# Kernel tuning notes

Measured on AMD Instinct MI355X. Metric: run time of the kernel, lower is better.

Reference implementation:

```python
import jax, jax.numpy as jnp
import numpy as np

N0, N1, N2 = 360448, 22528, 2048
E0, E1 = 337920, 20480
D = 256


def setup_inputs() -> dict:
    key = jax.random.key(0)
    ks = jax.random.split(key, 12)
    s = 1.0 / np.sqrt(D)
    return {
        "x": jax.random.normal(ks[0], (N0, D), dtype=jnp.float32),
        "src0": jax.random.randint(ks[1], (E0,), 0, N0, dtype=jnp.int32),
        "dst0": jax.random.randint(ks[2], (E0,), 0, N1, dtype=jnp.int32),
        "src1": jax.random.randint(ks[3], (E1,), 0, N1, dtype=jnp.int32),
        "dst1": jax.random.randint(ks[4], (E1,), 0, N2, dtype=jnp.int32),
        "Wl0": jax.random.normal(ks[5], (D, D), dtype=jnp.float32) * s,
        "bl0": jnp.zeros((D,), dtype=jnp.float32),
        "Wr0": jax.random.normal(ks[6], (D, D), dtype=jnp.float32) * s,
        "Wl1": jax.random.normal(ks[7], (D, D), dtype=jnp.float32) * s,
        "bl1": jnp.zeros((D,), dtype=jnp.float32),
        "Wr1": jax.random.normal(ks[8], (D, D), dtype=jnp.float32) * s,
    }


def _sage_conv(x_src, x_tgt, src, dst, n_tgt, Wl, bl, Wr):
    # mean aggregation of source neighbor features per target node
    summed = jax.ops.segment_sum(x_src[src], dst, num_segments=n_tgt)
    cnt = jax.ops.segment_sum(jnp.ones((src.shape[0],), x_src.dtype), dst,
                              num_segments=n_tgt)
    agg = summed / jnp.maximum(cnt, 1.0)[:, None]
    # PyG SAGEConv: lin_l(agg) + lin_r(x_target); lin_r has no bias
    return agg @ Wl.T + bl + x_tgt @ Wr.T


def reference(x, src0, dst0, src1, dst1, Wl0, bl0, Wr0, Wl1, bl1, Wr1):
    # layer 0: [N0, D] -> [N1, D]
    h = _sage_conv(x, x[:N1], src0, dst0, N1, Wl0, bl0, Wr0)
    h = jax.nn.relu(h)  # dropout is identity in eval mode
    # layer 1: [N1, D] -> [N2, D]
    out = _sage_conv(h, h[:N2], src1, dst1, N2, Wl1, bl1, Wr1)
    return out
```

## Files before the change

### kernel.cpp

```cpp
#include <hip/hip_runtime.h>
#include <hip/hip_bf16.h>

#define N1C 22528
#define N2C 2048

typedef __attribute__((ext_vector_type(8))) short bf16x8;
typedef __attribute__((ext_vector_type(4))) float f32x4;

__device__ __forceinline__ short f2bf(float f) {
    union { float f; unsigned u; } x; x.f = f;
    unsigned r = x.u + 0x7fff + ((x.u >> 16) & 1);
    return (short)(r >> 16);
}
__device__ __forceinline__ float bf2f(unsigned short u) {
    union { unsigned u; float f; } x; x.u = ((unsigned)u) << 16;
    return x.f;
}

__global__ void prep_kernel(const float* __restrict__ Wl0, const float* __restrict__ Wr0,
                            const float* __restrict__ Wl1, const float* __restrict__ Wr1,
                            short* __restrict__ Wcat0, short* __restrict__ Wcat1,
                            int* __restrict__ hist0, int* __restrict__ hist1) {
    const int stride = gridDim.x * blockDim.x;
    const int tid0 = blockIdx.x * blockDim.x + threadIdx.x;
    for (int i = tid0; i < 2 * 256 * 512; i += stride) {
        int layer = i >> 17;
        int r = i & ((1 << 17) - 1);
        int j = r >> 9, k = r & 511;
        const float* Wl = layer ? Wl1 : Wl0;
        const float* Wr = layer ? Wr1 : Wr0;
        float v = (k < 256) ? Wl[j * 256 + k] : Wr[j * 256 + (k - 256)];
        (layer ? Wcat1 : Wcat0)[r] = f2bf(v);
    }
    for (int i = tid0; i < N1C + N2C; i += stride) {
        if (i < N1C) hist0[i] = 0; else hist1[i - N1C] = 0;
    }
}

__global__ void hist_both_kernel(const int* __restrict__ dst0, int E0,
                                 const int* __restrict__ dst1, int E1,
                                 int* __restrict__ hist0, int* __restrict__ hist1) {
    const int stride = gridDim.x * blockDim.x;
    for (int i = blockIdx.x * blockDim.x + threadIdx.x; i < E0 + E1; i += stride) {
        if (i < E0) atomicAdd(&hist0[dst0[i]], 1);
        else        atomicAdd(&hist1[dst1[i - E0]], 1);
    }
}

__global__ __launch_bounds__(1024)
void scan_both_kernel(const int* __restrict__ hist0, int* __restrict__ rowptr0,
                      int* __restrict__ cursor0,
                      const int* __restrict__ hist1, int* __restrict__ rowptr1,
                      int* __restrict__ cursor1) {
    __shared__ int sums[1024];
    const int N = (blockIdx.x == 0) ? N1C : N2C;
    const int* hist   = (blockIdx.x == 0) ? hist0 : hist1;
    int* rowptr       = (blockIdx.x == 0) ? rowptr0 : rowptr1;
    int* cursor       = (blockIdx.x == 0) ? cursor0 : cursor1;
    const int tid = threadIdx.x;
    const int per = (N + 1023) >> 10;
    const int start = tid * per;
    const int end = min(start + per, N);
    int s = 0;
    for (int i = start; i < end; ++i) s += hist[i];
    sums[tid] = s;
    __syncthreads();
    for (int d = 1; d < 1024; d <<= 1) {
        int t = (tid >= d) ? sums[tid - d] : 0;
        __syncthreads();
        sums[tid] += t;
        __syncthreads();
    }
    int off = sums[tid] - s;
    for (int i = start; i < end; ++i) {
        rowptr[i] = off;
        cursor[i] = off;
        off += hist[i];
    }
    if (tid == 1023) rowptr[N] = off;
}

__global__ void fill_both_kernel(const int* __restrict__ src0, const int* __restrict__ dst0, int E0,
                                 const int* __restrict__ src1, const int* __restrict__ dst1, int E1,
                                 int* __restrict__ cursor0, int* __restrict__ eidx0,
                                 int* __restrict__ cursor1, int* __restrict__ eidx1) {
    const int stride = gridDim.x * blockDim.x;
    for (int i = blockIdx.x * blockDim.x + threadIdx.x; i < E0 + E1; i += stride) {
        if (i < E0) {
            int p = atomicAdd(&cursor0[dst0[i]], 1);
            eidx0[p] = src0[i];
        } else {
            int p = atomicAdd(&cursor1[dst1[i - E0]], 1);
            eidx1[p] = src1[i - E0];
        }
    }
}

__global__ __launch_bounds__(256)
void gather0_kernel(const float* __restrict__ x, const int* __restrict__ rowptr,
                    const int* __restrict__ eidx, short* __restrict__ Acat0) {
    const int wv = (blockIdx.x * 256 + threadIdx.x) >> 6;
    const int lane = threadIdx.x & 63;
    if (wv >= N1C) return;

    const float4 xr = *(const float4*)(x + (size_t)wv * 256 + lane * 4);

    const int beg = rowptr[wv];
    const int end = rowptr[wv + 1];
    float4 acc = {0.f, 0.f, 0.f, 0.f};
    float4 acc2 = {0.f, 0.f, 0.f, 0.f};
    int j = beg;
    for (; j + 3 < end; j += 4) {
        const int e0 = eidx[j], e1 = eidx[j + 1], e2 = eidx[j + 2], e3 = eidx[j + 3];
        const float4 v0 = *(const float4*)(x + (size_t)e0 * 256 + lane * 4);
        const float4 v1 = *(const float4*)(x + (size_t)e1 * 256 + lane * 4);
        const float4 v2 = *(const float4*)(x + (size_t)e2 * 256 + lane * 4);
        const float4 v3 = *(const float4*)(x + (size_t)e3 * 256 + lane * 4);
        acc.x += v0.x + v1.x;  acc.y += v0.y + v1.y;
        acc.z += v0.z + v1.z;  acc.w += v0.w + v1.w;
        acc2.x += v2.x + v3.x; acc2.y += v2.y + v3.y;
        acc2.z += v2.z + v3.z; acc2.w += v2.w + v3.w;
    }
    for (; j < end; ++j) {
        const float4 v0 = *(const float4*)(x + (size_t)eidx[j] * 256 + lane * 4);
        acc.x += v0.x; acc.y += v0.y; acc.z += v0.z; acc.w += v0.w;
    }
    acc.x += acc2.x; acc.y += acc2.y; acc.z += acc2.z; acc.w += acc2.w;

    const float sc = 1.0f / fmaxf((float)(end - beg), 1.0f);
    short4 o;
    o.x = f2bf(acc.x * sc); o.y = f2bf(acc.y * sc);
    o.z = f2bf(acc.z * sc); o.w = f2bf(acc.w * sc);
    *(short4*)(Acat0 + (size_t)wv * 512 + lane * 4) = o;

    short4 xo;
    xo.x = f2bf(xr.x); xo.y = f2bf(xr.y); xo.z = f2bf(xr.z); xo.w = f2bf(xr.w);
    *(short4*)(Acat0 + (size_t)wv * 512 + 256 + lane * 4) = xo;
}

__global__ __launch_bounds__(256)
void gather1_kernel(const ushort* __restrict__ X, const int* __restrict__ rowptr,
                    const int* __restrict__ eidx, short* __restrict__ Acat, int N) {
    const int wv = (blockIdx.x * 256 + threadIdx.x) >> 6;
    const int lane = threadIdx.x & 63;
    if (wv >= N) return;
    const int beg = rowptr[wv];
    const int end = rowptr[wv + 1];
    float a0 = 0.f, a1 = 0.f, a2 = 0.f, a3 = 0.f;
    int j = beg;
    for (; j + 1 < end; j += 2) {
        int s0 = eidx[j], s1 = eidx[j + 1];
        ushort4 v0 = *(const ushort4*)(X + (size_t)s0 * 256 + lane * 4);
        ushort4 v1 = *(const ushort4*)(X + (size_t)s1 * 256 + lane * 4);
        a0 += bf2f(v0.x) + bf2f(v1.x); a1 += bf2f(v0.y) + bf2f(v1.y);
        a2 += bf2f(v0.z) + bf2f(v1.z); a3 += bf2f(v0.w) + bf2f(v1.w);
    }
    if (j < end) {
        ushort4 v0 = *(const ushort4*)(X + (size_t)eidx[j] * 256 + lane * 4);
        a0 += bf2f(v0.x); a1 += bf2f(v0.y); a2 += bf2f(v0.z); a3 += bf2f(v0.w);
    }
    const float sc = 1.0f / fmaxf((float)(end - beg), 1.0f);
    short4 o;
    o.x = f2bf(a0 * sc); o.y = f2bf(a1 * sc);
    o.z = f2bf(a2 * sc); o.w = f2bf(a3 * sc);
    *(short4*)(Acat + (size_t)wv * 512 + lane * 4) = o;
}

template <int CT, bool RELU, bool OUT_BF16>
__global__ __launch_bounds__(256)
void mfma_gemm_kernel(const short* __restrict__ A, const short* __restrict__ W,
                      const float* __restrict__ bias, void* __restrict__ out,
                      short* __restrict__ out2, int M) {
    const int tid = threadIdx.x;
    const int wave = tid >> 6;
    const int lane = tid & 63;
    const int r0 = blockIdx.x * 64 + wave * 16;
    const int j0 = blockIdx.y * (CT * 16);
    const int lrow = lane & 15;
    const int lk = (lane >> 4) * 8;

    const short* arow = A + (size_t)(r0 + lrow) * 512 + lk;
    const short* wbase = W + (size_t)(j0 + lrow) * 512 + lk;

    f32x4 acc[CT] = {};
    for (int ks = 0; ks < 16; ++ks) {
        bf16x8 a = *(const bf16x8*)(arow + ks * 32);
#pragma unroll
        for (int c = 0; c < CT; ++c) {
            bf16x8 b = *(const bf16x8*)(wbase + (size_t)c * 16 * 512 + ks * 32);
            acc[c] = __builtin_amdgcn_mfma_f32_16x16x32_bf16(a, b, acc[c], 0, 0, 0);
        }
    }

    const int orow = (lane >> 4) * 4;
#pragma unroll
    for (int c = 0; c < CT; ++c) {
        const int col = j0 + c * 16 + lrow;
        const float bv = bias[col];
#pragma unroll
        for (int i = 0; i < 4; ++i) {
            const int row = r0 + orow + i;
            float v = acc[c][i] + bv;
            if (RELU) v = fmaxf(v, 0.0f);
            if (OUT_BF16) {
                short hv = f2bf(v);
                ((short*)out)[(size_t)row * 256 + col] = hv;
                if (out2 != nullptr && row < N2C)
                    out2[(size_t)row * 512 + 256 + col] = hv;
            } else {
                ((float*)out)[(size_t)row * 256 + col] = v;
            }
        }
    }
}

extern "C" void kernel_launch(void* const* d_in, const int* in_sizes, int n_in,
                              void* d_out, int out_size, void* d_ws, size_t ws_size,
                              hipStream_t stream) {
    const float* x    = (const float*)d_in[0];
    const int*   src0 = (const int*)d_in[1];
    const int*   dst0 = (const int*)d_in[2];
    const int*   src1 = (const int*)d_in[3];
    const int*   dst1 = (const int*)d_in[4];
    const float* Wl0  = (const float*)d_in[5];
    const float* bl0  = (const float*)d_in[6];
    const float* Wr0  = (const float*)d_in[7];
    const float* Wl1  = (const float*)d_in[8];
    const float* bl1  = (const float*)d_in[9];
    const float* Wr1  = (const float*)d_in[10];

    const int E0 = in_sizes[1];
    const int E1 = in_sizes[3];

    char* p = (char*)d_ws;
    short* Acat0 = (short*)p;            p += (size_t)N1C * 512 * 2;
    short* h     = (short*)p;            p += (size_t)N1C * 256 * 2;
    short* Acat1 = (short*)p;            p += (size_t)N2C * 512 * 2;
    short* Wcat0 = (short*)p;            p += 256 * 512 * 2;
    short* Wcat1 = (short*)p;            p += 256 * 512 * 2;
    int* hist0   = (int*)p;              p += (size_t)N1C * 4;
    int* cursor0 = (int*)p;              p += (size_t)N1C * 4;
    int* rowptr0 = (int*)p;              p += (size_t)(N1C + 4) * 4;
    int* hist1   = (int*)p;              p += (size_t)N2C * 4;
    int* cursor1 = (int*)p;              p += (size_t)N2C * 4;
    int* rowptr1 = (int*)p;              p += (size_t)(N2C + 4) * 4;
    int* eidx0   = (int*)p;              p += (size_t)E0 * 4;
    int* eidx1   = (int*)p;              p += (size_t)E1 * 4;

    prep_kernel<<<512, 256, 0, stream>>>(Wl0, Wr0, Wl1, Wr1, Wcat0, Wcat1, hist0, hist1);
    hist_both_kernel<<<512, 256, 0, stream>>>(dst0, E0, dst1, E1, hist0, hist1);
    scan_both_kernel<<<2, 1024, 0, stream>>>(hist0, rowptr0, cursor0, hist1, rowptr1, cursor1);
    fill_both_kernel<<<512, 256, 0, stream>>>(src0, dst0, E0, src1, dst1, E1,
                                              cursor0, eidx0, cursor1, eidx1);
    gather0_kernel<<<(N1C * 64 + 255) / 256, 256, 0, stream>>>(x, rowptr0, eidx0, Acat0);
    mfma_gemm_kernel<16, true, true><<<dim3(N1C / 64, 1), 256, 0, stream>>>(
        Acat0, Wcat0, bl0, h, Acat1, N1C);
    gather1_kernel<<<(N2C * 64 + 255) / 256, 256, 0, stream>>>(
        (const ushort*)h, rowptr1, eidx1, Acat1, N2C);
    mfma_gemm_kernel<4, false, false><<<dim3(N2C / 64, 4), 256, 0, stream>>>(
        Acat1, Wcat1, bl1, (float*)d_out, nullptr, N2C);
}
```

Measured before the change: 231.7 us.

## Use wave-shuffle scan, deeper gather unroll, and split layer-0 GEMM columns

The block scan now uses wave shuffles plus a small per-wave sum array instead of a 10-step shared-memory Hillis-Steele loop with many barriers. The layer-0 gather unrolls to 8 neighbor loads in flight, which raises memory-level parallelism. The GEMM k-loop is fully unrolled, and the layer-0 GEMM is split into 4 column tiles of 64 instead of one 256-wide tile, giving four times as many blocks and fewer accumulators per wave. In exchange, each A tile is now loaded from global memory four times.

```diff
diff --git a/kernel.cpp b/kernel.cpp
--- a/kernel.cpp
+++ b/kernel.cpp
@@ -1,6 +1,7 @@
 #include <hip/hip_runtime.h>
 #include <hip/hip_bf16.h>
 
+#define N0C 360448
 #define N1C 22528
 #define N2C 2048
 
@@ -17,13 +18,14 @@
     return x.f;
 }
 
-__global__ void prep_kernel(const float* __restrict__ Wl0, const float* __restrict__ Wr0,
-                            const float* __restrict__ Wl1, const float* __restrict__ Wr1,
-                            short* __restrict__ Wcat0, short* __restrict__ Wcat1,
-                            int* __restrict__ hist0, int* __restrict__ hist1) {
+__global__ __launch_bounds__(256)
+void prep_kernel(const float* __restrict__ Wl0, const float* __restrict__ Wr0,
+                 const float* __restrict__ Wl1, const float* __restrict__ Wr1,
+                 short* __restrict__ Wcat0, short* __restrict__ Wcat1,
+                 int* __restrict__ hist0, int* __restrict__ hist1) {
     const int stride = gridDim.x * blockDim.x;
-    const int tid0 = blockIdx.x * blockDim.x + threadIdx.x;
-    for (int i = tid0; i < 2 * 256 * 512; i += stride) {
+    const int t0 = blockIdx.x * blockDim.x + threadIdx.x;
+    for (int i = t0; i < 2 * 256 * 512; i += stride) {
         int layer = i >> 17;
         int r = i & ((1 << 17) - 1);
         int j = r >> 9, k = r & 511;
@@ -32,7 +34,7 @@
         float v = (k < 256) ? Wl[j * 256 + k] : Wr[j * 256 + (k - 256)];
         (layer ? Wcat1 : Wcat0)[r] = f2bf(v);
     }
-    for (int i = tid0; i < N1C + N2C; i += stride) {
+    for (int i = t0; i < N1C + N2C; i += stride) {
         if (i < N1C) hist0[i] = 0; else hist1[i - N1C] = 0;
     }
 }
@@ -52,32 +54,44 @@
                       int* __restrict__ cursor0,
                       const int* __restrict__ hist1, int* __restrict__ rowptr1,
                       int* __restrict__ cursor1) {
-    __shared__ int sums[1024];
+    __shared__ int wsum[16];
     const int N = (blockIdx.x == 0) ? N1C : N2C;
     const int* hist   = (blockIdx.x == 0) ? hist0 : hist1;
     int* rowptr       = (blockIdx.x == 0) ? rowptr0 : rowptr1;
     int* cursor       = (blockIdx.x == 0) ? cursor0 : cursor1;
     const int tid = threadIdx.x;
+    const int lane = tid & 63;
+    const int wid = tid >> 6;
     const int per = (N + 1023) >> 10;
-    const int start = tid * per;
+    const int start = min(tid * per, N);
     const int end = min(start + per, N);
     int s = 0;
     for (int i = start; i < end; ++i) s += hist[i];
-    sums[tid] = s;
+    int incl = s;
+#pragma unroll
+    for (int d = 1; d < 64; d <<= 1) {
+        int t = __shfl_up(incl, d);
+        if (lane >= d) incl += t;
+    }
+    if (lane == 63) wsum[wid] = incl;
     __syncthreads();
-    for (int d = 1; d < 1024; d <<= 1) {
-        int t = (tid >= d) ? sums[tid - d] : 0;
-        __syncthreads();
-        sums[tid] += t;
-        __syncthreads();
-    }
-    int off = sums[tid] - s;
+    if (wid == 0) {
+        int v = (lane < 16) ? wsum[lane] : 0;
+#pragma unroll
+        for (int d = 1; d < 16; d <<= 1) {
+            int t = __shfl_up(v, d);
+            if (lane >= d) v += t;
+        }
+        if (lane < 16) wsum[lane] = v;
+    }
+    __syncthreads();
+    int off = (wid > 0 ? wsum[wid - 1] : 0) + (incl - s);
     for (int i = start; i < end; ++i) {
         rowptr[i] = off;
         cursor[i] = off;
         off += hist[i];
     }
-    if (tid == 1023) rowptr[N] = off;
+    if (tid == 1023) rowptr[N] = wsum[15];
 }
 
 __global__ void fill_both_kernel(const int* __restrict__ src0, const int* __restrict__ dst0, int E0,
@@ -102,40 +116,45 @@
     const int wv = (blockIdx.x * 256 + threadIdx.x) >> 6;
     const int lane = threadIdx.x & 63;
     if (wv >= N1C) return;
-
-    const float4 xr = *(const float4*)(x + (size_t)wv * 256 + lane * 4);
+    const int co = lane * 4;
+
+    const float4 xr = *(const float4*)(x + (size_t)wv * 256 + co);
 
     const int beg = rowptr[wv];
     const int end = rowptr[wv + 1];
-    float4 acc = {0.f, 0.f, 0.f, 0.f};
-    float4 acc2 = {0.f, 0.f, 0.f, 0.f};
+    f32x4 acc = {0.f, 0.f, 0.f, 0.f};
+    f32x4 acc2 = {0.f, 0.f, 0.f, 0.f};
     int j = beg;
-    for (; j + 3 < end; j += 4) {
-        const int e0 = eidx[j], e1 = eidx[j + 1], e2 = eidx[j + 2], e3 = eidx[j + 3];
-        const float4 v0 = *(const float4*)(x + (size_t)e0 * 256 + lane * 4);
-        const float4 v1 = *(const float4*)(x + (size_t)e1 * 256 + lane * 4);
-        const float4 v2 = *(const float4*)(x + (size_t)e2 * 256 + lane * 4);
-        const float4 v3 = *(const float4*)(x + (size_t)e3 * 256 + lane * 4);
-        acc.x += v0.x + v1.x;  acc.y += v0.y + v1.y;
-        acc.z += v0.z + v1.z;  acc.w += v0.w + v1.w;
-        acc2.x += v2.x + v3.x; acc2.y += v2.y + v3.y;
-        acc2.z += v2.z + v3.z; acc2.w += v2.w + v3.w;
-    }
-    for (; j < end; ++j) {
-        const float4 v0 = *(const float4*)(x + (size_t)eidx[j] * 256 + lane * 4);
-        acc.x += v0.x; acc.y += v0.y; acc.z += v0.z; acc.w += v0.w;
-    }
-    acc.x += acc2.x; acc.y += acc2.y; acc.z += acc2.z; acc.w += acc2.w;
+    for (; j + 7 < end; j += 8) {
+        const f32x4 v0 = *(const f32x4*)(x + (size_t)eidx[j    ] * 256 + co);
+        const f32x4 v1 = *(const f32x4*)(x + (size_t)eidx[j + 1] * 256 + co);
+        const f32x4 v2 = *(const f32x4*)(x + (size_t)eidx[j + 2] * 256 + co);
+        const f32x4 v3 = *(const f32x4*)(x + (size_t)eidx[j + 3] * 256 + co);
+        const f32x4 v4 = *(const f32x4*)(x + (size_t)eidx[j + 4] * 256 + co);
+        const f32x4 v5 = *(const f32x4*)(x + (size_t)eidx[j + 5] * 256 + co);
+        const f32x4 v6 = *(const f32x4*)(x + (size_t)eidx[j + 6] * 256 + co);
+        const f32x4 v7 = *(const f32x4*)(x + (size_t)eidx[j + 7] * 256 + co);
+        acc  += v0 + v1 + v2 + v3;
+        acc2 += v4 + v5 + v6 + v7;
+    }
+    for (; j + 1 < end; j += 2) {
+        const f32x4 v0 = *(const f32x4*)(x + (size_t)eidx[j    ] * 256 + co);
+        const f32x4 v1 = *(const f32x4*)(x + (size_t)eidx[j + 1] * 256 + co);
+        acc += v0 + v1;
+    }
+    if (j < end)
+        acc2 += *(const f32x4*)(x + (size_t)eidx[j] * 256 + co);
+    acc += acc2;
 
     const float sc = 1.0f / fmaxf((float)(end - beg), 1.0f);
     short4 o;
     o.x = f2bf(acc.x * sc); o.y = f2bf(acc.y * sc);
     o.z = f2bf(acc.z * sc); o.w = f2bf(acc.w * sc);
-    *(short4*)(Acat0 + (size_t)wv * 512 + lane * 4) = o;
+    *(short4*)(Acat0 + (size_t)wv * 512 + co) = o;
 
     short4 xo;
     xo.x = f2bf(xr.x); xo.y = f2bf(xr.y); xo.z = f2bf(xr.z); xo.w = f2bf(xr.w);
-    *(short4*)(Acat0 + (size_t)wv * 512 + 256 + lane * 4) = xo;
+    *(short4*)(Acat0 + (size_t)wv * 512 + 256 + co) = xo;
 }
 
 __global__ __launch_bounds__(256)
@@ -183,6 +202,7 @@
     const short* wbase = W + (size_t)(j0 + lrow) * 512 + lk;
 
     f32x4 acc[CT] = {};
+#pragma unroll
     for (int ks = 0; ks < 16; ++ks) {
         bf16x8 a = *(const bf16x8*)(arow + ks * 32);
 #pragma unroll
@@ -253,7 +273,7 @@
     fill_both_kernel<<<512, 256, 0, stream>>>(src0, dst0, E0, src1, dst1, E1,
                                               cursor0, eidx0, cursor1, eidx1);
     gather0_kernel<<<(N1C * 64 + 255) / 256, 256, 0, stream>>>(x, rowptr0, eidx0, Acat0);
-    mfma_gemm_kernel<16, true, true><<<dim3(N1C / 64, 1), 256, 0, stream>>>(
+    mfma_gemm_kernel<4, true, true><<<dim3(N1C / 64, 4), 256, 0, stream>>>(
         Acat0, Wcat0, bl0, h, Acat1, N1C);
     gather1_kernel<<<(N2C * 64 + 255) / 256, 256, 0, stream>>>(
         (const ushort*)h, rowptr1, eidx1, Acat1, N2C);
```

After: 221.3 us. -4.5%, faster.
